# Performance work log

Hardware: AMD Instinct MI355X
Metric: run time of the kernel (lower is better)

The kernel has to match this reference:

```python
import jax, jax.numpy as jnp
import numpy as np

B = 131072          # points on manifold
A = 16              # n_anchors
SDIM = 512          # substrate.n (spatial dim); ambient dim = SDIM + 1
ALPHA = 0.1         # attraction coefficient
EPS = 1e-7


def _proj(p):
    # Project onto hyperboloid: recompute time coord from spatial part.
    sp = p[..., 1:]
    t = jnp.sqrt(1.0 + jnp.sum(sp * sp, axis=-1, keepdims=True))
    return jnp.concatenate([t, sp], axis=-1)


def _linner(x, y):
    # Lorentz inner product <x,y>_L = -x0*y0 + sum_i xi*yi
    return -x[..., 0] * y[..., 0] + jnp.sum(x[..., 1:] * y[..., 1:], axis=-1)


def setup_inputs() -> dict:
    key = jax.random.key(0)
    k1, k2 = jax.random.split(key)
    x_sp = jax.random.normal(k1, (B, SDIM), dtype=jnp.float32)
    x = _proj(jnp.concatenate([jnp.zeros((B, 1), jnp.float32), x_sp], axis=-1))
    a_sp = jax.random.normal(k2, (A, SDIM), dtype=jnp.float32) * 0.01
    anchors = _proj(jnp.concatenate([jnp.zeros((A, 1), jnp.float32), a_sp], axis=-1))
    return {"x": x, "anchors": anchors}


def reference(x, anchors):
    af = _proj(anchors)                                   # [A, D]
    D = af.shape[-1]
    metric = jnp.concatenate([-jnp.ones((1,), x.dtype), jnp.ones((D - 1,), x.dtype)])
    # pairwise -<x,a>_L  -> [B, A]
    theta_all = -jnp.einsum('bd,ad->ba', x * metric, af)
    dists = jnp.arccosh(jnp.clip(theta_all, 1.0 + EPS, None))
    idx = jnp.argmin(dists, axis=1)                       # nearest anchor per point
    y = af[idx]                                           # [B, D]
    # log_map_x(y) = acosh(theta)/sqrt(theta^2-1) * (y - theta*x)
    theta = jnp.clip(-_linner(x, y), 1.0 + EPS, None)[:, None]
    direction = (jnp.arccosh(theta) / jnp.sqrt(theta * theta - 1.0)) * (y - theta * x)
    v = ALPHA * direction                                 # tangent vector
    # exp_map_x(v) = cosh(||v||_L) x + sinh(||v||_L)/||v||_L * v
    vn = jnp.sqrt(jnp.clip(_linner(v, v), EPS, None))[:, None]
    return jnp.cosh(vn) * x + (jnp.sinh(vn) / vn) * v
```

## Files before the change

kernel.cpp:

```cpp
#include <hip/hip_runtime.h>

#define NA 16
#define DD 513
#define ALPHA 0.1f
#define EPSV 1e-7f
#define RPW 16
#define GRID 2048

typedef __fp16 h2 __attribute__((ext_vector_type(2)));
typedef unsigned int u32;

union H2U { h2 h; u32 u; };

static __device__ __forceinline__ u32 pkrtz(float lo, float hi) {
    H2U t; t.h = __builtin_amdgcn_cvt_pkrtz(lo, hi); return t.u;
}
static __device__ __forceinline__ h2 asH2(u32 w) { H2U t; t.u = w; return t.h; }

static __device__ __forceinline__ float fdot2(u32 a, u32 b, float c) {
#if __has_builtin(__builtin_amdgcn_fdot2)
    return __builtin_amdgcn_fdot2(asH2(a), asH2(b), c, false);
#else
    h2 ha = asH2(a), hb = asH2(b);
    c = fmaf((float)ha.x, (float)hb.x, c);
    return fmaf((float)ha.y, (float)hb.y, c);
#endif
}

#define RSTEP(m, half)                                              \
    _Pragma("unroll")                                               \
    for (int i = 0; i < half; ++i) {                                \
        const bool up = (lane & m) != 0;                            \
        float snd = up ? v[i] : v[half + i];                        \
        float kp  = up ? v[half + i] : v[i];                        \
        v[i] = kp + __shfl_xor(snd, m);                             \
    }

static __device__ __forceinline__ float reduce16(float v[16], int lane) {
    RSTEP(1, 8)
    RSTEP(2, 4)
    RSTEP(4, 2)
    RSTEP(8, 1)
    float S = v[0];
    S += __shfl_xor(S, 16);
    S += __shfl_xor(S, 32);
    return S;
}

__global__ __launch_bounds__(256, 4)
void hfield_kernel(const float* __restrict__ x,
                   const float* __restrict__ anc,
                   float* __restrict__ out) {
    __shared__ u32 ah[NA][64][4];

    const int tid = threadIdx.x, lane = tid & 63, wid = tid >> 6;

    for (int i = tid; i < NA * 256; i += 256) {
        const int a = i >> 8, rem = i & 255, l = rem >> 2, k = rem & 3;
        ah[a][l][k] = pkrtz(anc[a * DD + 1 + l + 128 * k],
                            anc[a * DD + 1 + l + 64 + 128 * k]);
    }
    __syncthreads();

    const int aidx = ((lane & 1) << 3) | (((lane >> 1) & 1) << 2) |
                     (((lane >> 2) & 1) << 1) | ((lane >> 3) & 1);

    float af0;
    {
        float v[16];
#pragma unroll
        for (int a = 0; a < NA; ++a) {
            const uint4 w = *reinterpret_cast<const uint4*>(&ah[a][lane][0]);
            float s = fdot2(w.x, w.x, 0.f);
            s = fdot2(w.y, w.y, s);
            s = fdot2(w.z, w.z, s);
            v[a] = fdot2(w.w, w.w, s);
        }
        af0 = sqrtf(1.0f + reduce16(v, lane));
    }

    const int gw = blockIdx.x * 4 + wid;
    const float* rbase = x + (size_t)gw * RPW * DD;
    float*       obase = out + (size_t)gw * RPW * DD;

    float xa[8], xb[8];
    float x0a, x0b;
    {
        const float* p = rbase + 1 + lane;
#pragma unroll
        for (int j = 0; j < 8; ++j) xa[j] = p[64 * j];
        x0a = rbase[0];
        const float* q = rbase + DD + 1 + lane;
#pragma unroll
        for (int j = 0; j < 8; ++j) xb[j] = q[64 * j];
        x0b = rbase[DD];
    }

#pragma unroll 1
    for (int it = 0; it < RPW; ++it) {
        float xn[8] = {0, 0, 0, 0, 0, 0, 0, 0};
        float x0n = 0.f;
        if (it + 2 < RPW) {
            const float* p = rbase + (size_t)(it + 2) * DD;
            const float* ps = p + 1 + lane;
#pragma unroll
            for (int j = 0; j < 8; ++j) xn[j] = ps[64 * j];
            x0n = p[0];
        }

        const u32 xp0 = pkrtz(xa[0], xa[1]);
        const u32 xp1 = pkrtz(xa[2], xa[3]);
        const u32 xp2 = pkrtz(xa[4], xa[5]);
        const u32 xp3 = pkrtz(xa[6], xa[7]);

        float v[16];
#pragma unroll
        for (int a = 0; a < NA; ++a) {
            const uint4 w = *reinterpret_cast<const uint4*>(&ah[a][lane][0]);
            float s = fdot2(w.x, xp0, 0.f);
            s = fdot2(w.y, xp1, s);
            s = fdot2(w.z, xp2, s);
            v[a] = fdot2(w.w, xp3, s);
        }
        const float S = reduce16(v, lane);

        float tc = fmaxf(fmaf(x0a, af0, -S), 1.0f + 1e-7f);
        int idx = aidx;
#pragma unroll
        for (int m = 1; m <= 8; m <<= 1) {
            float vo = __shfl_xor(tc, m);
            int   io = __shfl_xor(idx, m);
            bool take = (vo < tc) || (vo == tc && io < idx);
            tc  = take ? vo : tc;
            idx = take ? io : idx;
        }
        const int bi = __builtin_amdgcn_readfirstlane(idx);

        const float s2   = tc * tc - 1.0f;
        const float rr   = sqrtf(s2);
        const float ach  = __logf(tc + rr);
        const float coef = ach / rr;
        const float vn   = sqrtf(fmaxf(ALPHA * ALPHA * ach * ach, EPSV));
        const float e    = __expf(vn);
        const float ei   = 1.0f / e;
        const float ch   = 0.5f * (e + ei);
        const float sh   = 0.5f * (e - ei);
        const float c2   = ALPHA * coef * (sh / vn);
        const float c1   = fmaf(-c2, tc, ch);

        const uint4 wy = *reinterpret_cast<const uint4*>(&ah[bi][lane][0]);
        float yv[8];
        { h2 t = asH2(wy.x); yv[0] = (float)t.x; yv[1] = (float)t.y; }
        { h2 t = asH2(wy.y); yv[2] = (float)t.x; yv[3] = (float)t.y; }
        { h2 t = asH2(wy.z); yv[4] = (float)t.x; yv[5] = (float)t.y; }
        { h2 t = asH2(wy.w); yv[6] = (float)t.x; yv[7] = (float)t.y; }

        float* op = obase + (size_t)it * DD;
        float* sp = op + 1 + lane;
#pragma unroll
        for (int j = 0; j < 8; ++j)
            __builtin_nontemporal_store(fmaf(c2, yv[j], c1 * xa[j]), &sp[64 * j]);

        const int lsrc = ((bi >> 3) & 1) | (((bi >> 2) & 1) << 1) |
                         (((bi >> 1) & 1) << 2) | ((bi & 1) << 3);
        const float y0 = __shfl(af0, lsrc);
        if (lane == 0)
            __builtin_nontemporal_store(fmaf(c2, y0, c1 * x0a), op);

#pragma unroll
        for (int j = 0; j < 8; ++j) { xa[j] = xb[j]; xb[j] = xn[j]; }
        x0a = x0b; x0b = x0n;
    }
}

extern "C" void kernel_launch(void* const* d_in, const int* in_sizes, int n_in,
                              void* d_out, int out_size, void* d_ws, size_t ws_size,
                              hipStream_t stream) {
    const float* x   = (const float*)d_in[0];
    const float* anc = (const float*)d_in[1];
    float* out       = (float*)d_out;
    hipLaunchKernelGGL(hfield_kernel, dim3(GRID), dim3(256), 0, stream, x, anc, out);
}
```

Baseline: 124.7 us.

## Process two rows per iteration with packed-key argmin and halved rows per wave

Each loop iteration now handles two rows, interleaving their fdot2 chains and shuffle reductions for more ILP. The argmin packs the anchor index into the low mantissa bits of theta, so each butterfly step is one shuffle and one unsigned min. The winning theta is then fetched by a shuffle. Rows per wave are halved and the grid doubled to keep total work the same. The packed key can pick a slightly different anchor on near-ties, prefetch depth becomes one row pair, and register pressure rises.

```diff
diff --git a/kernel.cpp b/kernel.cpp
--- a/kernel.cpp
+++ b/kernel.cpp
@@ -4,13 +4,14 @@
 #define DD 513
 #define ALPHA 0.1f
 #define EPSV 1e-7f
-#define RPW 16
-#define GRID 2048
+#define RPW 8
+#define GRID 4096
 
 typedef __fp16 h2 __attribute__((ext_vector_type(2)));
 typedef unsigned int u32;
 
 union H2U { h2 h; u32 u; };
+union FU  { float f; u32 u; };
 
 static __device__ __forceinline__ u32 pkrtz(float lo, float hi) {
     H2U t; t.h = __builtin_amdgcn_cvt_pkrtz(lo, hi); return t.u;
@@ -18,34 +19,20 @@
 static __device__ __forceinline__ h2 asH2(u32 w) { H2U t; t.u = w; return t.h; }
 
 static __device__ __forceinline__ float fdot2(u32 a, u32 b, float c) {
-#if __has_builtin(__builtin_amdgcn_fdot2)
     return __builtin_amdgcn_fdot2(asH2(a), asH2(b), c, false);
-#else
-    h2 ha = asH2(a), hb = asH2(b);
-    c = fmaf((float)ha.x, (float)hb.x, c);
-    return fmaf((float)ha.y, (float)hb.y, c);
-#endif
-}
-
-#define RSTEP(m, half)                                              \
+}
+
+#define RSTEP2(m, half)                                             \
     _Pragma("unroll")                                               \
     for (int i = 0; i < half; ++i) {                                \
         const bool up = (lane & m) != 0;                            \
-        float snd = up ? v[i] : v[half + i];                        \
-        float kp  = up ? v[half + i] : v[i];                        \
-        v[i] = kp + __shfl_xor(snd, m);                             \
-    }
-
-static __device__ __forceinline__ float reduce16(float v[16], int lane) {
-    RSTEP(1, 8)
-    RSTEP(2, 4)
-    RSTEP(4, 2)
-    RSTEP(8, 1)
-    float S = v[0];
-    S += __shfl_xor(S, 16);
-    S += __shfl_xor(S, 32);
-    return S;
-}
+        float s0 = up ? v0[i] : v0[half + i];                       \
+        float k0 = up ? v0[half + i] : v0[i];                       \
+        float s1 = up ? v1[i] : v1[half + i];                       \
+        float k1 = up ? v1[half + i] : v1[i];                       \
+        v0[i] = k0 + __shfl_xor(s0, m);                             \
+        v1[i] = k1 + __shfl_xor(s1, m);                             \
+    }
 
 __global__ __launch_bounds__(256, 4)
 void hfield_kernel(const float* __restrict__ x,
@@ -67,109 +54,147 @@
 
     float af0;
     {
-        float v[16];
+        float v0[16], v1[16];
 #pragma unroll
         for (int a = 0; a < NA; ++a) {
             const uint4 w = *reinterpret_cast<const uint4*>(&ah[a][lane][0]);
             float s = fdot2(w.x, w.x, 0.f);
             s = fdot2(w.y, w.y, s);
             s = fdot2(w.z, w.z, s);
-            v[a] = fdot2(w.w, w.w, s);
-        }
-        af0 = sqrtf(1.0f + reduce16(v, lane));
+            v0[a] = fdot2(w.w, w.w, s);
+            v1[a] = 0.f;
+        }
+        RSTEP2(1, 8) RSTEP2(2, 4) RSTEP2(4, 2) RSTEP2(8, 1)
+        float S = v0[0];
+        S += __shfl_xor(S, 16);
+        S += __shfl_xor(S, 32);
+        af0 = sqrtf(1.0f + S);
     }
 
     const int gw = blockIdx.x * 4 + wid;
     const float* rbase = x + (size_t)gw * RPW * DD;
     float*       obase = out + (size_t)gw * RPW * DD;
 
-    float xa[8], xb[8];
-    float x0a, x0b;
+    float xc0[8], xc1[8], x00, x01;
     {
-        const float* p = rbase + 1 + lane;
-#pragma unroll
-        for (int j = 0; j < 8; ++j) xa[j] = p[64 * j];
-        x0a = rbase[0];
-        const float* q = rbase + DD + 1 + lane;
-#pragma unroll
-        for (int j = 0; j < 8; ++j) xb[j] = q[64 * j];
-        x0b = rbase[DD];
+        const float* p0 = rbase;
+        const float* p1 = rbase + DD;
+#pragma unroll
+        for (int j = 0; j < 8; ++j) xc0[j] = p0[1 + lane + 64 * j];
+        x00 = p0[0];
+#pragma unroll
+        for (int j = 0; j < 8; ++j) xc1[j] = p1[1 + lane + 64 * j];
+        x01 = p1[0];
     }
 
 #pragma unroll 1
-    for (int it = 0; it < RPW; ++it) {
-        float xn[8] = {0, 0, 0, 0, 0, 0, 0, 0};
-        float x0n = 0.f;
-        if (it + 2 < RPW) {
-            const float* p = rbase + (size_t)(it + 2) * DD;
-            const float* ps = p + 1 + lane;
-#pragma unroll
-            for (int j = 0; j < 8; ++j) xn[j] = ps[64 * j];
-            x0n = p[0];
-        }
-
-        const u32 xp0 = pkrtz(xa[0], xa[1]);
-        const u32 xp1 = pkrtz(xa[2], xa[3]);
-        const u32 xp2 = pkrtz(xa[4], xa[5]);
-        const u32 xp3 = pkrtz(xa[6], xa[7]);
-
-        float v[16];
+    for (int it = 0; it < RPW / 2; ++it) {
+        float xn0[8] = {0,0,0,0,0,0,0,0}, xn1[8] = {0,0,0,0,0,0,0,0};
+        float x0n0 = 0.f, x0n1 = 0.f;
+        if (it + 1 < RPW / 2) {
+            const float* p0 = rbase + (size_t)(2 * it + 2) * DD;
+            const float* p1 = p0 + DD;
+#pragma unroll
+            for (int j = 0; j < 8; ++j) xn0[j] = p0[1 + lane + 64 * j];
+            x0n0 = p0[0];
+#pragma unroll
+            for (int j = 0; j < 8; ++j) xn1[j] = p1[1 + lane + 64 * j];
+            x0n1 = p1[0];
+        }
+
+        const u32 a0 = pkrtz(xc0[0], xc0[1]), a1 = pkrtz(xc0[2], xc0[3]);
+        const u32 a2 = pkrtz(xc0[4], xc0[5]), a3 = pkrtz(xc0[6], xc0[7]);
+        const u32 b0 = pkrtz(xc1[0], xc1[1]), b1 = pkrtz(xc1[2], xc1[3]);
+        const u32 b2 = pkrtz(xc1[4], xc1[5]), b3 = pkrtz(xc1[6], xc1[7]);
+
+        float v0[16], v1[16];
 #pragma unroll
         for (int a = 0; a < NA; ++a) {
             const uint4 w = *reinterpret_cast<const uint4*>(&ah[a][lane][0]);
-            float s = fdot2(w.x, xp0, 0.f);
-            s = fdot2(w.y, xp1, s);
-            s = fdot2(w.z, xp2, s);
-            v[a] = fdot2(w.w, xp3, s);
-        }
-        const float S = reduce16(v, lane);
-
-        float tc = fmaxf(fmaf(x0a, af0, -S), 1.0f + 1e-7f);
-        int idx = aidx;
+            float s0 = fdot2(w.x, a0, 0.f);
+            float s1 = fdot2(w.x, b0, 0.f);
+            s0 = fdot2(w.y, a1, s0);
+            s1 = fdot2(w.y, b1, s1);
+            s0 = fdot2(w.z, a2, s0);
+            s1 = fdot2(w.z, b2, s1);
+            v0[a] = fdot2(w.w, a3, s0);
+            v1[a] = fdot2(w.w, b3, s1);
+        }
+
+        RSTEP2(1, 8) RSTEP2(2, 4) RSTEP2(4, 2) RSTEP2(8, 1)
+        float S0 = v0[0], S1 = v1[0];
+        S0 += __shfl_xor(S0, 16);  S1 += __shfl_xor(S1, 16);
+        S0 += __shfl_xor(S0, 32);  S1 += __shfl_xor(S1, 32);
+
+        const float tc0 = fmaxf(fmaf(x00, af0, -S0), 1.0f + 1e-7f);
+        const float tc1 = fmaxf(fmaf(x01, af0, -S1), 1.0f + 1e-7f);
+
+        FU u0, u1; u0.f = tc0; u1.f = tc1;
+        u32 k0 = (u0.u & 0xFFFFFFF0u) | (u32)aidx;
+        u32 k1 = (u1.u & 0xFFFFFFF0u) | (u32)aidx;
 #pragma unroll
         for (int m = 1; m <= 8; m <<= 1) {
-            float vo = __shfl_xor(tc, m);
-            int   io = __shfl_xor(idx, m);
-            bool take = (vo < tc) || (vo == tc && io < idx);
-            tc  = take ? vo : tc;
-            idx = take ? io : idx;
-        }
-        const int bi = __builtin_amdgcn_readfirstlane(idx);
-
-        const float s2   = tc * tc - 1.0f;
-        const float rr   = sqrtf(s2);
-        const float ach  = __logf(tc + rr);
-        const float coef = ach / rr;
-        const float vn   = sqrtf(fmaxf(ALPHA * ALPHA * ach * ach, EPSV));
-        const float e    = __expf(vn);
-        const float ei   = 1.0f / e;
-        const float ch   = 0.5f * (e + ei);
-        const float sh   = 0.5f * (e - ei);
-        const float c2   = ALPHA * coef * (sh / vn);
-        const float c1   = fmaf(-c2, tc, ch);
-
-        const uint4 wy = *reinterpret_cast<const uint4*>(&ah[bi][lane][0]);
-        float yv[8];
-        { h2 t = asH2(wy.x); yv[0] = (float)t.x; yv[1] = (float)t.y; }
-        { h2 t = asH2(wy.y); yv[2] = (float)t.x; yv[3] = (float)t.y; }
-        { h2 t = asH2(wy.z); yv[4] = (float)t.x; yv[5] = (float)t.y; }
-        { h2 t = asH2(wy.w); yv[6] = (float)t.x; yv[7] = (float)t.y; }
-
-        float* op = obase + (size_t)it * DD;
-        float* sp = op + 1 + lane;
-#pragma unroll
-        for (int j = 0; j < 8; ++j)
-            __builtin_nontemporal_store(fmaf(c2, yv[j], c1 * xa[j]), &sp[64 * j]);
-
-        const int lsrc = ((bi >> 3) & 1) | (((bi >> 2) & 1) << 1) |
-                         (((bi >> 1) & 1) << 2) | ((bi & 1) << 3);
-        const float y0 = __shfl(af0, lsrc);
-        if (lane == 0)
-            __builtin_nontemporal_store(fmaf(c2, y0, c1 * x0a), op);
-
-#pragma unroll
-        for (int j = 0; j < 8; ++j) { xa[j] = xb[j]; xb[j] = xn[j]; }
-        x0a = x0b; x0b = x0n;
+            const u32 o0 = (u32)__shfl_xor((int)k0, m);
+            const u32 o1 = (u32)__shfl_xor((int)k1, m);
+            k0 = o0 < k0 ? o0 : k0;
+            k1 = o1 < k1 ? o1 : k1;
+        }
+        const int bi0 = __builtin_amdgcn_readfirstlane((int)(k0 & 15u));
+        const int bi1 = __builtin_amdgcn_readfirstlane((int)(k1 & 15u));
+
+        const int ls0 = ((bi0 >> 3) & 1) | (((bi0 >> 2) & 1) << 1) |
+                        (((bi0 >> 1) & 1) << 2) | ((bi0 & 1) << 3);
+        const int ls1 = ((bi1 >> 3) & 1) | (((bi1 >> 2) & 1) << 1) |
+                        (((bi1 >> 1) & 1) << 2) | ((bi1 & 1) << 3);
+        const float t0 = __shfl(tc0, ls0);
+        const float t1 = __shfl(tc1, ls1);
+        const float y00 = __shfl(af0, ls0);
+        const float y01 = __shfl(af0, ls1);
+
+        const float s20 = t0 * t0 - 1.0f,  s21 = t1 * t1 - 1.0f;
+        const float rr0 = sqrtf(s20),      rr1 = sqrtf(s21);
+        const float ac0 = __logf(t0 + rr0), ac1 = __logf(t1 + rr1);
+        const float cf0 = ac0 / rr0,        cf1 = ac1 / rr1;
+        const float vn0 = sqrtf(fmaxf(ALPHA * ALPHA * ac0 * ac0, EPSV));
+        const float vn1 = sqrtf(fmaxf(ALPHA * ALPHA * ac1 * ac1, EPSV));
+        const float e0 = __expf(vn0),  e1 = __expf(vn1);
+        const float i0 = 1.0f / e0,    i1 = 1.0f / e1;
+        const float ch0 = 0.5f * (e0 + i0), ch1 = 0.5f * (e1 + i1);
+        const float sh0 = 0.5f * (e0 - i0), sh1 = 0.5f * (e1 - i1);
+        const float c20 = ALPHA * cf0 * (sh0 / vn0);
+        const float c21 = ALPHA * cf1 * (sh1 / vn1);
+        const float c10 = fmaf(-c20, t0, ch0);
+        const float c11 = fmaf(-c21, t1, ch1);
+
+        const uint4 wy0 = *reinterpret_cast<const uint4*>(&ah[bi0][lane][0]);
+        const uint4 wy1 = *reinterpret_cast<const uint4*>(&ah[bi1][lane][0]);
+        float yv0[8], yv1[8];
+        { h2 t = asH2(wy0.x); yv0[0] = (float)t.x; yv0[1] = (float)t.y; }
+        { h2 t = asH2(wy0.y); yv0[2] = (float)t.x; yv0[3] = (float)t.y; }
+        { h2 t = asH2(wy0.z); yv0[4] = (float)t.x; yv0[5] = (float)t.y; }
+        { h2 t = asH2(wy0.w); yv0[6] = (float)t.x; yv0[7] = (float)t.y; }
+        { h2 t = asH2(wy1.x); yv1[0] = (float)t.x; yv1[1] = (float)t.y; }
+        { h2 t = asH2(wy1.y); yv1[2] = (float)t.x; yv1[3] = (float)t.y; }
+        { h2 t = asH2(wy1.z); yv1[4] = (float)t.x; yv1[5] = (float)t.y; }
+        { h2 t = asH2(wy1.w); yv1[6] = (float)t.x; yv1[7] = (float)t.y; }
+
+        float* op0 = obase + (size_t)(2 * it) * DD;
+        float* op1 = op0 + DD;
+#pragma unroll
+        for (int j = 0; j < 8; ++j) {
+            __builtin_nontemporal_store(fmaf(c20, yv0[j], c10 * xc0[j]),
+                                        &op0[1 + lane + 64 * j]);
+            __builtin_nontemporal_store(fmaf(c21, yv1[j], c11 * xc1[j]),
+                                        &op1[1 + lane + 64 * j]);
+        }
+        if (lane == 0) {
+            __builtin_nontemporal_store(fmaf(c20, y00, c10 * x00), op0);
+            __builtin_nontemporal_store(fmaf(c21, y01, c11 * x01), op1);
+        }
+
+#pragma unroll
+        for (int j = 0; j < 8; ++j) { xc0[j] = xn0[j]; xc1[j] = xn1[j]; }
+        x00 = x0n0; x01 = x0n1;
     }
 }
 
```

After: 187.6 us. 1.5x slower.

## Compute anchor inner products with MFMA 16x16x32 f16 and a two-pass row scheme

Applied to the files above, without the earlier changes.

Replaces the per-row fdot2 dot products and 16-way shuffle reduction with MFMA 16x16x32 f16 matrix instructions, working on 16 rows per tile against all 16 anchors. Argmin now uses a packed key (theta bits with the anchor index in the low 4 bits). Per-row coefficients are passed through shared memory, and a second pass re-reads x to write the outputs. Each row is therefore read twice from global memory, which trades extra bandwidth or cache traffic for less ALU work. The key packing also drops the low mantissa bits of theta when breaking ties between close anchors.

```diff
diff --git a/kernel.cpp b/kernel.cpp
--- a/kernel.cpp
+++ b/kernel.cpp
@@ -4,172 +4,150 @@
 #define DD 513
 #define ALPHA 0.1f
 #define EPSV 1e-7f
-#define RPW 16
-#define GRID 2048
+#define TPW 2
+#define GRID 1024
 
 typedef __fp16 h2 __attribute__((ext_vector_type(2)));
+typedef __fp16 f16x8 __attribute__((ext_vector_type(8)));
+typedef float f32x4 __attribute__((ext_vector_type(4)));
 typedef unsigned int u32;
 
 union H2U { h2 h; u32 u; };
+union FU  { float f; u32 u; int i; };
+union FRAG { u32 w[4]; f16x8 v; };
 
 static __device__ __forceinline__ u32 pkrtz(float lo, float hi) {
     H2U t; t.h = __builtin_amdgcn_cvt_pkrtz(lo, hi); return t.u;
 }
 static __device__ __forceinline__ h2 asH2(u32 w) { H2U t; t.u = w; return t.h; }
 
-static __device__ __forceinline__ float fdot2(u32 a, u32 b, float c) {
-#if __has_builtin(__builtin_amdgcn_fdot2)
-    return __builtin_amdgcn_fdot2(asH2(a), asH2(b), c, false);
-#else
-    h2 ha = asH2(a), hb = asH2(b);
-    c = fmaf((float)ha.x, (float)hb.x, c);
-    return fmaf((float)ha.y, (float)hb.y, c);
-#endif
-}
+struct __attribute__((packed, aligned(4))) F4 { float a, b, c, d; };
 
-#define RSTEP(m, half)                                              \
-    _Pragma("unroll")                                               \
-    for (int i = 0; i < half; ++i) {                                \
-        const bool up = (lane & m) != 0;                            \
-        float snd = up ? v[i] : v[half + i];                        \
-        float kp  = up ? v[half + i] : v[i];                        \
-        v[i] = kp + __shfl_xor(snd, m);                             \
-    }
-
-static __device__ __forceinline__ float reduce16(float v[16], int lane) {
-    RSTEP(1, 8)
-    RSTEP(2, 4)
-    RSTEP(4, 2)
-    RSTEP(8, 1)
-    float S = v[0];
-    S += __shfl_xor(S, 16);
-    S += __shfl_xor(S, 32);
-    return S;
-}
-
-__global__ __launch_bounds__(256, 4)
+__global__ __launch_bounds__(256, 2)
 void hfield_kernel(const float* __restrict__ x,
                    const float* __restrict__ anc,
                    float* __restrict__ out) {
     __shared__ u32 ah[NA][64][4];
+    __shared__ u32 bh[16][64][4];
+    __shared__ float parts[NA][16];
+    __shared__ float af_s[NA];
+    __shared__ float4 cb[4][16];
 
     const int tid = threadIdx.x, lane = tid & 63, wid = tid >> 6;
+    const int col = lane & 15, g = lane >> 4;
 
     for (int i = tid; i < NA * 256; i += 256) {
         const int a = i >> 8, rem = i & 255, l = rem >> 2, k = rem & 3;
         ah[a][l][k] = pkrtz(anc[a * DD + 1 + l + 128 * k],
                             anc[a * DD + 1 + l + 64 + 128 * k]);
     }
+    for (int i = tid; i < 16 * 256; i += 256) {
+        const int kt = i >> 8, rem = i & 255, l = rem >> 2, q = rem & 3;
+        const float* p = anc + (l & 15) * DD + 1 + kt * 32 + (l >> 4) * 8 + 2 * q;
+        bh[kt][l][q] = pkrtz(p[0], p[1]);
+    }
+    {
+        const int a = tid >> 4, seg = tid & 15;
+        const float* p = anc + a * DD + 1 + seg * 32;
+        float s = 0.f;
+#pragma unroll
+        for (int i = 0; i < 32; ++i) s = fmaf(p[i], p[i], s);
+        parts[a][seg] = s;
+    }
+    __syncthreads();
+    if (tid < NA) {
+        float s = 0.f;
+#pragma unroll
+        for (int i = 0; i < 16; ++i) s += parts[tid][i];
+        af_s[tid] = sqrtf(1.0f + s);
+    }
     __syncthreads();
 
-    const int aidx = ((lane & 1) << 3) | (((lane >> 1) & 1) << 2) |
-                     (((lane >> 2) & 1) << 1) | ((lane >> 3) & 1);
-
-    float af0;
-    {
-        float v[16];
-#pragma unroll
-        for (int a = 0; a < NA; ++a) {
-            const uint4 w = *reinterpret_cast<const uint4*>(&ah[a][lane][0]);
-            float s = fdot2(w.x, w.x, 0.f);
-            s = fdot2(w.y, w.y, s);
-            s = fdot2(w.z, w.z, s);
-            v[a] = fdot2(w.w, w.w, s);
-        }
-        af0 = sqrtf(1.0f + reduce16(v, lane));
-    }
-
+    const float af0c = af_s[col];
+    const float thmin = 1.0f + 1e-7f;
     const int gw = blockIdx.x * 4 + wid;
-    const float* rbase = x + (size_t)gw * RPW * DD;
-    float*       obase = out + (size_t)gw * RPW * DD;
-
-    float xa[8], xb[8];
-    float x0a, x0b;
-    {
-        const float* p = rbase + 1 + lane;
-#pragma unroll
-        for (int j = 0; j < 8; ++j) xa[j] = p[64 * j];
-        x0a = rbase[0];
-        const float* q = rbase + DD + 1 + lane;
-#pragma unroll
-        for (int j = 0; j < 8; ++j) xb[j] = q[64 * j];
-        x0b = rbase[DD];
-    }
 
 #pragma unroll 1
-    for (int it = 0; it < RPW; ++it) {
-        float xn[8] = {0, 0, 0, 0, 0, 0, 0, 0};
-        float x0n = 0.f;
-        if (it + 2 < RPW) {
-            const float* p = rbase + (size_t)(it + 2) * DD;
-            const float* ps = p + 1 + lane;
+    for (int t = 0; t < TPW; ++t) {
+        const int rowbase = gw * (16 * TPW) + t * 16;
+
+        const float* arow = x + (size_t)(rowbase + col) * DD + 1 + g * 8;
+        f32x4 acc = {0.f, 0.f, 0.f, 0.f};
 #pragma unroll
-            for (int j = 0; j < 8; ++j) xn[j] = ps[64 * j];
-            x0n = p[0];
+        for (int kt = 0; kt < 16; ++kt) {
+            const F4 lo = *(const F4*)(arow + kt * 32);
+            const F4 hi = *(const F4*)(arow + kt * 32 + 4);
+            FRAG A, Bf;
+            A.w[0] = pkrtz(lo.a, lo.b); A.w[1] = pkrtz(lo.c, lo.d);
+            A.w[2] = pkrtz(hi.a, hi.b); A.w[3] = pkrtz(hi.c, hi.d);
+            const uint4 bw = *reinterpret_cast<const uint4*>(&bh[kt][lane][0]);
+            Bf.w[0] = bw.x; Bf.w[1] = bw.y; Bf.w[2] = bw.z; Bf.w[3] = bw.w;
+            acc = __builtin_amdgcn_mfma_f32_16x16x32_f16(A.v, Bf.v, acc, 0, 0, 0);
         }
 
-        const u32 xp0 = pkrtz(xa[0], xa[1]);
-        const u32 xp1 = pkrtz(xa[2], xa[3]);
-        const u32 xp2 = pkrtz(xa[4], xa[5]);
-        const u32 xp3 = pkrtz(xa[6], xa[7]);
-
-        float v[16];
+        float x0r[4];
 #pragma unroll
-        for (int a = 0; a < NA; ++a) {
-            const uint4 w = *reinterpret_cast<const uint4*>(&ah[a][lane][0]);
-            float s = fdot2(w.x, xp0, 0.f);
-            s = fdot2(w.y, xp1, s);
-            s = fdot2(w.z, xp2, s);
-            v[a] = fdot2(w.w, xp3, s);
-        }
-        const float S = reduce16(v, lane);
-
-        float tc = fmaxf(fmaf(x0a, af0, -S), 1.0f + 1e-7f);
-        int idx = aidx;
-#pragma unroll
-        for (int m = 1; m <= 8; m <<= 1) {
-            float vo = __shfl_xor(tc, m);
-            int   io = __shfl_xor(idx, m);
-            bool take = (vo < tc) || (vo == tc && io < idx);
-            tc  = take ? vo : tc;
-            idx = take ? io : idx;
-        }
-        const int bi = __builtin_amdgcn_readfirstlane(idx);
-
-        const float s2   = tc * tc - 1.0f;
-        const float rr   = sqrtf(s2);
-        const float ach  = __logf(tc + rr);
-        const float coef = ach / rr;
-        const float vn   = sqrtf(fmaxf(ALPHA * ALPHA * ach * ach, EPSV));
-        const float e    = __expf(vn);
-        const float ei   = 1.0f / e;
-        const float ch   = 0.5f * (e + ei);
-        const float sh   = 0.5f * (e - ei);
-        const float c2   = ALPHA * coef * (sh / vn);
-        const float c1   = fmaf(-c2, tc, ch);
-
-        const uint4 wy = *reinterpret_cast<const uint4*>(&ah[bi][lane][0]);
-        float yv[8];
-        { h2 t = asH2(wy.x); yv[0] = (float)t.x; yv[1] = (float)t.y; }
-        { h2 t = asH2(wy.y); yv[2] = (float)t.x; yv[3] = (float)t.y; }
-        { h2 t = asH2(wy.z); yv[4] = (float)t.x; yv[5] = (float)t.y; }
-        { h2 t = asH2(wy.w); yv[6] = (float)t.x; yv[7] = (float)t.y; }
-
-        float* op = obase + (size_t)it * DD;
-        float* sp = op + 1 + lane;
-#pragma unroll
-        for (int j = 0; j < 8; ++j)
-            __builtin_nontemporal_store(fmaf(c2, yv[j], c1 * xa[j]), &sp[64 * j]);
-
-        const int lsrc = ((bi >> 3) & 1) | (((bi >> 2) & 1) << 1) |
-                         (((bi >> 1) & 1) << 2) | ((bi & 1) << 3);
-        const float y0 = __shfl(af0, lsrc);
-        if (lane == 0)
-            __builtin_nontemporal_store(fmaf(c2, y0, c1 * x0a), op);
+        for (int r4 = 0; r4 < 4; ++r4)
+            x0r[r4] = x[(size_t)(rowbase + 4 * g + r4) * DD];
 
 #pragma unroll
-        for (int j = 0; j < 8; ++j) { xa[j] = xb[j]; xb[j] = xn[j]; }
-        x0a = x0b; x0b = x0n;
+        for (int r4 = 0; r4 < 4; ++r4) {
+            const float th = fmaxf(fmaf(x0r[r4], af0c, -acc[r4]), thmin);
+            FU u; u.f = th;
+            u32 key = (u.u & 0xFFFFFFF0u) | (u32)col;
+#pragma unroll
+            for (int m = 1; m <= 8; m <<= 1) {
+                const u32 o = (u32)__shfl_xor((int)key, m);
+                key = o < key ? o : key;
+            }
+            const int bi  = (int)(key & 15u);
+            const int src = (lane & 48) | bi;
+            const float thw = __shfl(th, src);
+            const float y0  = af_s[bi];
+
+            const float s2 = thw * thw - 1.0f;
+            const float rr = sqrtf(s2);
+            const float ac = __logf(thw + rr);
+            const float cf = ac / rr;
+            const float vn = sqrtf(fmaxf(ALPHA * ALPHA * ac * ac, EPSV));
+            const float e  = __expf(vn);
+            const float ei = 1.0f / e;
+            const float ch = 0.5f * (e + ei);
+            const float sh = 0.5f * (e - ei);
+            const float c2 = ALPHA * cf * (sh / vn);
+            const float c1 = fmaf(-c2, thw, ch);
+
+            if (col == 0) {
+                FU bf; bf.i = bi;
+                cb[wid][4 * g + r4] = make_float4(c1, c2, y0, bf.f);
+            }
+        }
+        asm volatile("s_waitcnt lgkmcnt(0)" ::: "memory");
+
+#pragma unroll 4
+        for (int r = 0; r < 16; ++r) {
+            const float4 c = cb[wid][r];
+            FU bu; bu.f = c.w;
+            const int bi = bu.i;
+            const uint4 wy = *reinterpret_cast<const uint4*>(&ah[bi][lane][0]);
+            const float* px = x + (size_t)(rowbase + r) * DD;
+            float xv[8];
+#pragma unroll
+            for (int j = 0; j < 8; ++j) xv[j] = px[1 + lane + 64 * j];
+            float yv[8];
+            { h2 tt = asH2(wy.x); yv[0] = (float)tt.x; yv[1] = (float)tt.y; }
+            { h2 tt = asH2(wy.y); yv[2] = (float)tt.x; yv[3] = (float)tt.y; }
+            { h2 tt = asH2(wy.z); yv[4] = (float)tt.x; yv[5] = (float)tt.y; }
+            { h2 tt = asH2(wy.w); yv[6] = (float)tt.x; yv[7] = (float)tt.y; }
+
+            float* op = out + (size_t)(rowbase + r) * DD;
+            const float out0 = fmaf(c.y, c.z, c.x * px[0]);
+            if (lane == 0) __builtin_nontemporal_store(out0, op);
+#pragma unroll
+            for (int j = 0; j < 8; ++j)
+                __builtin_nontemporal_store(fmaf(c.y, yv[j], c.x * xv[j]),
+                                            &op[1 + lane + 64 * j]);
+        }
     }
 }
 
```

New measurement: 139.9 us. 1.12x slower.
